# Kernel optimization log

Measured on AMD Instinct MI355X. Metric: run time of the kernel, lower is better.

Reference implementation:

```python
import jax, jax.numpy as jnp
import numpy as np

B, T, D, H, HD, FF, L, M = 2, 1024, 1024, 16, 64, 4096, 4, 128


def _ln(x, g, b):
    m = x.mean(-1, keepdims=True)
    v = ((x - m) ** 2).mean(-1, keepdims=True)
    return (x - m) * jax.lax.rsqrt(v + 1e-5) * g + b


def _rope(x, cos, sin):
    # x: (B,H,T,HD) viewed as interleaved (even,odd) pairs, as in torch Rotary
    xp = x.reshape(x.shape[:-1] + (HD // 2, 2))
    x1, x2 = xp[..., 0], xp[..., 1]
    even = x1 * cos - x2 * sin
    odd = x1 * sin + x2 * cos
    return jnp.stack([even, odd], -1).reshape(x.shape)


def setup_inputs() -> dict:
    key = jax.random.key(0)
    ks = iter(jax.random.split(key, 16))

    def n(shape, s=0.02):
        return jax.random.normal(next(ks), shape, jnp.float32) * s

    return {
        'x': jax.random.normal(next(ks), (B, T, D), jnp.float32),
        'context': jax.random.normal(next(ks), (B, T, D), jnp.float32),
        'W_in': n((D, D)), 'b_in': jnp.zeros((D,), jnp.float32),
        'ln_in_g': jnp.ones((D,), jnp.float32), 'ln_in_b': jnp.zeros((D,), jnp.float32),
        'ln1_g': jnp.ones((L, D), jnp.float32), 'ln1_b': jnp.zeros((L, D), jnp.float32),
        'Wqkv': n((L, D, 3 * D)), 'bqkv': jnp.zeros((L, 3 * D), jnp.float32),
        'Wproj': n((L, D, D)), 'bproj': jnp.zeros((L, D), jnp.float32),
        'rel_bias': n((L, 2 * M + 1, H)),
        'ln2_g': jnp.ones((L, D), jnp.float32), 'ln2_b': jnp.zeros((L, D), jnp.float32),
        'Wfc1': n((L, D, 2 * FF)), 'bfc1': jnp.zeros((L, 2 * FF), jnp.float32),
        'Wfc2': n((L, FF, D)), 'bfc2': jnp.zeros((L, D), jnp.float32),
        'ln_f_g': jnp.ones((D,), jnp.float32), 'ln_f_b': jnp.zeros((D,), jnp.float32),
        'W_out': n((D, D)), 'b_out': jnp.zeros((D,), jnp.float32),
        'alpha': jnp.array([0.3], jnp.float32),
        'beta': jnp.zeros((1,), jnp.float32),
        'alpha_scale': jnp.array([0.5], jnp.float32),
        'beta_scale': jnp.array([0.1], jnp.float32),
    }


def reference(x, context, W_in, b_in, ln_in_g, ln_in_b, ln1_g, ln1_b, Wqkv, bqkv,
              Wproj, bproj, rel_bias, ln2_g, ln2_b, Wfc1, bfc1, Wfc2, bfc2,
              ln_f_g, ln_f_b, W_out, b_out, alpha, beta, alpha_scale, beta_scale):
    scale = HD ** -0.5
    # Rotary cache (replicates the torch code's emb=cat(freqs,freqs) then
    # view(T, HD//2, 2)[...,0] quirk exactly)
    t = jnp.arange(T, dtype=jnp.float32)
    inv_freq = 1.0 / (10000.0 ** (jnp.arange(0, HD, 2, dtype=jnp.float32) / HD))
    emb = jnp.concatenate([jnp.outer(t, inv_freq)] * 2, -1)  # (T, HD)
    cos = jnp.cos(emb).reshape(T, HD // 2, 2)[..., 0]        # (T, HD/2)
    sin = jnp.sin(emb).reshape(T, HD // 2, 2)[..., 0]
    # relative-position index (T,T), clamped to [-M, M]
    idx = jnp.arange(T)
    rel = jnp.clip(idx[None, :] - idx[:, None], -M, M) + M

    h = _ln(x @ W_in + b_in + context, ln_in_g, ln_in_b)

    def step(h, p):
        g1, b1, wqkv, bq, wp, bp, rb, g2, b2, w1, bf1, w2, bf2 = p
        hn = _ln(h, g1, b1)
        qkv = (hn @ wqkv + bq).reshape(B, T, 3, H, HD)
        q = jnp.moveaxis(qkv[:, :, 0], 1, 2)   # (B,H,T,HD)
        k = jnp.moveaxis(qkv[:, :, 1], 1, 2)
        v = jnp.moveaxis(qkv[:, :, 2], 1, 2)
        q = _rope(q, cos, sin)
        k = _rope(k, cos, sin)
        bias = rb[rel].transpose(2, 0, 1)      # (H,T,T)
        attn = jax.nn.softmax(jnp.einsum('bhqd,bhkd->bhqk', q, k) * scale + bias[None], -1)
        out = jnp.einsum('bhqk,bhkd->bhqd', attn, v)
        out = jnp.moveaxis(out, 1, 2).reshape(B, T, D) @ wp + bp
        h = h + out
        hn2 = _ln(h, g2, b2)
        ab = hn2 @ w1 + bf1
        a, gate = ab[..., :FF], ab[..., FF:]
        h = h + (a * jax.nn.gelu(gate, approximate=False)) @ w2 + bf2
        return h, None

    h, _ = jax.lax.scan(step, h, (ln1_g, ln1_b, Wqkv, bqkv, Wproj, bproj, rel_bias,
                                  ln2_g, ln2_b, Wfc1, bfc1, Wfc2, bfc2))
    h = _ln(h, ln_f_g, ln_f_b)
    o = h @ W_out + b_out
    # MotionAmplifier
    a_s = jnp.clip(alpha_scale, 0.0, 1.0)
    ms = jnp.linalg.norm(o, axis=-1, keepdims=True)
    sc = 1.0 + alpha * a_s * jnp.minimum(ms, 5.0)
    return jnp.clip(o * sc + beta * beta_scale, -10.0, 10.0) + o
```

## Files before the change

### kernel.cpp

```cpp
#include <hip/hip_runtime.h>
#include <cmath>

#define B_  2
#define T_  1024
#define D_  1024
#define H_  16
#define HD_ 64
#define FF_ 4096
#define L_  4
#define M_  128

typedef __bf16 bf16x8 __attribute__((ext_vector_type(8)));
typedef __bf16 bf16x4 __attribute__((ext_vector_type(4)));
typedef float f32x4 __attribute__((ext_vector_type(4)));

__device__ __forceinline__ void async16(const void* g, void* l) {
    __builtin_amdgcn_global_load_lds(
        (const __attribute__((address_space(1))) unsigned int*)g,
        (__attribute__((address_space(3))) unsigned int*)l, 16, 0, 0);
}

template<int BM, typename CT>
__global__ __launch_bounds__(256) void gemm_bf16(
    const __bf16* __restrict__ A, const __bf16* __restrict__ Wt,
    const float* __restrict__ bias, const float* __restrict__ res,
    CT* __restrict__ C, int M, int N, int K)
{
    constexpr int MI = BM / 32;
    __shared__ alignas(16) __bf16 As[BM * 32];
    __shared__ alignas(16) __bf16 Bs[128 * 32];

    const int tid  = threadIdx.x;
    const int lane = tid & 63;
    const int wave = tid >> 6;
    const int wm   = wave & 1;
    const int wn   = wave >> 1;
    const int quad = lane >> 4;
    const int l16  = lane & 15;
    const int m0   = blockIdx.y * BM;
    const int n0   = blockIdx.x * 128;

    f32x4 acc[MI][4];
    #pragma unroll
    for (int i = 0; i < MI; i++)
        #pragma unroll
        for (int j = 0; j < 4; j++) acc[i][j] = (f32x4){0.f, 0.f, 0.f, 0.f};

    for (int k0 = 0; k0 < K; k0 += 32) {
        #pragma unroll
        for (int i = 0; i < BM / 64; i++) {
            int off = (i * 256 + tid) * 16;
            int row = off >> 6, chunk = (off >> 4) & 3;
            int gcol = (chunk ^ ((row >> 1) & 3)) * 8;
            async16(A + (size_t)(m0 + row) * K + k0 + gcol,
                    (char*)As + i * 4096 + wave * 1024);
        }
        #pragma unroll
        for (int i = 0; i < 2; i++) {
            int off = (i * 256 + tid) * 16;
            int row = off >> 6, chunk = (off >> 4) & 3;
            int gcol = (chunk ^ ((row >> 1) & 3)) * 8;
            async16(Wt + (size_t)(n0 + row) * K + k0 + gcol,
                    (char*)Bs + i * 4096 + wave * 1024);
        }
        __syncthreads();

        bf16x8 af[MI], bfr[4];
        #pragma unroll
        for (int mi = 0; mi < MI; mi++) {
            int r = wm * (BM / 2) + mi * 16 + l16;
            af[mi] = *(const bf16x8*)((const char*)As + r * 64 + (quad ^ ((r >> 1) & 3)) * 16);
        }
        #pragma unroll
        for (int ni = 0; ni < 4; ni++) {
            int r = wn * 64 + ni * 16 + l16;
            bfr[ni] = *(const bf16x8*)((const char*)Bs + r * 64 + (quad ^ ((r >> 1) & 3)) * 16);
        }
        #pragma unroll
        for (int mi = 0; mi < MI; mi++)
            #pragma unroll
            for (int ni = 0; ni < 4; ni++)
                acc[mi][ni] = __builtin_amdgcn_mfma_f32_16x16x32_bf16(
                    af[mi], bfr[ni], acc[mi][ni], 0, 0, 0);
        __syncthreads();
    }

    #pragma unroll
    for (int mi = 0; mi < MI; mi++) {
        #pragma unroll
        for (int ni = 0; ni < 4; ni++) {
            int col = n0 + wn * 64 + ni * 16 + l16;
            #pragma unroll
            for (int r = 0; r < 4; r++) {
                int row = m0 + wm * (BM / 2) + mi * 16 + quad * 4 + r;
                float v = acc[mi][ni][r] + bias[col];
                if (res) v += res[(size_t)row * N + col];
                C[(size_t)row * N + col] = (CT)v;
            }
        }
    }
}

__global__ __launch_bounds__(256) void transpose_w_kernel(
    const float* __restrict__ W, __bf16* __restrict__ Wt, int K, int N)
{
    __shared__ __bf16 t[64][80];
    int n0 = blockIdx.x * 64, k0 = blockIdx.y * 64;
    int tid = threadIdx.x;
    int r = tid >> 2, cb = (tid & 3) * 16;
    const float* src = W + (size_t)(k0 + r) * N + n0 + cb;
    #pragma unroll
    for (int j = 0; j < 16; j += 4) {
        f32x4 v = *(const f32x4*)(src + j);
        #pragma unroll
        for (int u = 0; u < 4; u++) t[cb + j + u][r] = (__bf16)v[u];
    }
    __syncthreads();
    __bf16* dst = Wt + (size_t)(n0 + r) * K + k0 + cb;
    *(bf16x8*)(dst)     = *(const bf16x8*)&t[r][cb];
    *(bf16x8*)(dst + 8) = *(const bf16x8*)&t[r][cb + 8];
}

__global__ __launch_bounds__(256) void cvt_bf16_kernel(
    const float* __restrict__ in, __bf16* __restrict__ out)
{
    size_t i = ((size_t)blockIdx.x * 256 + threadIdx.x) * 8;
    f32x4 a = *(const f32x4*)(in + i);
    f32x4 b = *(const f32x4*)(in + i + 4);
    bf16x8 o;
    #pragma unroll
    for (int u = 0; u < 4; u++) { o[u] = (__bf16)a[u]; o[4 + u] = (__bf16)b[u]; }
    *(bf16x8*)(out + i) = o;
}

template<typename OT>
__global__ __launch_bounds__(256) void ln_kernel(
    const float* __restrict__ in,
    const float* __restrict__ g, const float* __restrict__ b,
    OT* __restrict__ out)
{
    int row = blockIdx.x;
    int t = threadIdx.x;
    __shared__ float red[256];
    __shared__ float red2[256];
    const float* ip = in + (size_t)row * D_;
    float v[4];
    float sum = 0.f, sumsq = 0.f;
    #pragma unroll
    for (int j = 0; j < 4; j++) {
        int c = t + j * 256;
        float x = ip[c];
        v[j] = x;
        sum += x; sumsq += x * x;
    }
    red[t] = sum; red2[t] = sumsq;
    __syncthreads();
    for (int s = 128; s > 0; s >>= 1) {
        if (t < s) { red[t] += red[t + s]; red2[t] += red2[t + s]; }
        __syncthreads();
    }
    float mean = red[0] * (1.0f / D_);
    float var  = red2[0] * (1.0f / D_) - mean * mean;
    float rstd = rsqrtf(var + 1e-5f);
    #pragma unroll
    for (int j = 0; j < 4; j++) {
        int c = t + j * 256;
        out[(size_t)row * D_ + c] = (OT)((v[j] - mean) * rstd * g[c] + b[c]);
    }
}

__global__ __launch_bounds__(256) void repack_kernel(
    const float* __restrict__ qkv, __bf16* __restrict__ qp,
    __bf16* __restrict__ kp, __bf16* __restrict__ vp)
{
    int bh = blockIdx.y; int h = bh & (H_ - 1); int b = bh >> 4;
    int t0 = blockIdx.x * 64;
    int tid = threadIdx.x;
    __shared__ float vt[64][65];

    int r  = tid >> 2;
    int tg = t0 + r;
    int pb = (tid & 3) * 8;
    #pragma unroll
    for (int j = 0; j < 8; j++) {
        int p = pb + j;
        int jj = (2 * p) & 31;
        float f = expf(-(float)jj * (9.210340371976184f / 32.0f));
        float ang = (float)tg * f;
        float c = cosf(ang), s = sinf(ang);
        const float2 xq = *(const float2*)(qkv + ((size_t)(b * T_ + tg) * 3 + 0) * D_ + h * HD_ + 2 * p);
        size_t oq = ((size_t)bh * T_ + tg) * HD_ + 2 * p;
        qp[oq]     = (__bf16)(xq.x * c - xq.y * s);
        qp[oq + 1] = (__bf16)(xq.x * s + xq.y * c);
        const float2 xk = *(const float2*)(qkv + ((size_t)(b * T_ + tg) * 3 + 1) * D_ + h * HD_ + 2 * p);
        kp[oq]     = (__bf16)(xk.x * c - xk.y * s);
        kp[oq + 1] = (__bf16)(xk.x * s + xk.y * c);
    }
    {
        int cb = (tid & 3) * 16;
        const float* vsrc = qkv + ((size_t)(b * T_ + tg) * 3 + 2) * D_ + h * HD_ + cb;
        #pragma unroll
        for (int j = 0; j < 16; j += 4) {
            f32x4 v = *(const f32x4*)(vsrc + j);
            #pragma unroll
            for (int u = 0; u < 4; u++) vt[cb + j + u][r] = v[u];
        }
    }
    __syncthreads();
    {
        int d = tid >> 2, cb = (tid & 3) * 16;
        bf16x8 o0, o1;
        #pragma unroll
        for (int u = 0; u < 8; u++) { o0[u] = (__bf16)vt[d][cb + u]; o1[u] = (__bf16)vt[d][cb + 8 + u]; }
        __bf16* dst = vp + ((size_t)bh * HD_ + d) * T_ + t0 + cb;
        *(bf16x8*)(dst) = o0;
        *(bf16x8*)(dst + 8) = o1;
    }
}

__global__ __launch_bounds__(256) void attn_mfma_kernel(
    const __bf16* __restrict__ qp, const __bf16* __restrict__ kp,
    const __bf16* __restrict__ vp, const float* __restrict__ rb,
    __bf16* __restrict__ out)
{
    int bh = blockIdx.y; int h = bh & (H_ - 1); int b = bh >> 4;
    int q0 = blockIdx.x * 64;
    int tid = threadIdx.x;
    int lane = tid & 63, wave = tid >> 6;
    int quad = lane >> 4, l16 = lane & 15;

    __shared__ alignas(16) __bf16 Qs[64 * 64];
    __shared__ alignas(16) __bf16 Ks[64 * 64];
    __shared__ alignas(16) __bf16 Vs[64 * 64];
    __shared__ __bf16 Ps[4][16][72];
    __shared__ float rbs[2 * M_ + 1];

    for (int i = tid; i < 2 * M_ + 1; i += 256) rbs[i] = rb[i * H_ + h];

    #pragma unroll
    for (int i = 0; i < 2; i++) {
        int off = (i * 256 + tid) * 16;
        int row = off >> 7, chunk = (off >> 4) & 7;
        int gcol = (chunk ^ (row & 7)) * 8;
        async16(qp + ((size_t)bh * T_ + q0 + row) * HD_ + gcol,
                (char*)Qs + i * 4096 + wave * 1024);
    }
    __syncthreads();

    bf16x8 qfrag[2];
    {
        int r = wave * 16 + l16;
        qfrag[0] = *(const bf16x8*)((const char*)Qs + r * 128 + ((quad)     ^ (r & 7)) * 16);
        qfrag[1] = *(const bf16x8*)((const char*)Qs + r * 128 + ((4 + quad) ^ (r & 7)) * 16);
    }

    float m_run[4], l_run[4];
    f32x4 o_acc[4];
    #pragma unroll
    for (int r2 = 0; r2 < 4; r2++) { m_run[r2] = -1e30f; l_run[r2] = 0.f; }
    #pragma unroll
    for (int ni = 0; ni < 4; ni++) o_acc[ni] = (f32x4){0.f, 0.f, 0.f, 0.f};

    const int row_l  = quad * 4;
    const int qrow_g = q0 + wave * 16 + row_l;

    for (int k0 = 0; k0 < T_; k0 += 64) {
        __syncthreads();
        #pragma unroll
        for (int i = 0; i < 2; i++) {
            int off = (i * 256 + tid) * 16;
            int row = off >> 7, chunk = (off >> 4) & 7;
            int gcol = (chunk ^ (row & 7)) * 8;
            async16(kp + ((size_t)bh * T_ + k0 + row) * HD_ + gcol,
                    (char*)Ks + i * 4096 + wave * 1024);
            async16(vp + ((size_t)bh * HD_ + row) * T_ + k0 + gcol,
                    (char*)Vs + i * 4096 + wave * 1024);
        }
        __syncthreads();

        f32x4 s_acc[4];
        #pragma unroll
        for (int ni = 0; ni < 4; ni++) s_acc[ni] = (f32x4){0.f, 0.f, 0.f, 0.f};
        #pragma unroll
        for (int ni = 0; ni < 4; ni++) {
            int r = ni * 16 + l16;
            bf16x8 kf0 = *(const bf16x8*)((const char*)Ks + r * 128 + ((quad)     ^ (r & 7)) * 16);
            bf16x8 kf1 = *(const bf16x8*)((const char*)Ks + r * 128 + ((4 + quad) ^ (r & 7)) * 16);
            s_acc[ni] = __builtin_amdgcn_mfma_f32_16x16x32_bf16(qfrag[0], kf0, s_acc[ni], 0, 0, 0);
            s_acc[ni] = __builtin_amdgcn_mfma_f32_16x16x32_bf16(qfrag[1], kf1, s_acc[ni], 0, 0, 0);
        }

        float sv[4][4];
        float rmax[4] = {-1e30f, -1e30f, -1e30f, -1e30f};
        #pragma unroll
        for (int ni = 0; ni < 4; ni++) {
            int colg = k0 + ni * 16 + l16;
            #pragma unroll
            for (int r2 = 0; r2 < 4; r2++) {
                int rel = colg - (qrow_g + r2);
                rel = (rel < -M_) ? -M_ : (rel > M_ ? M_ : rel);
                float s = s_acc[ni][r2] * 0.125f + rbs[rel + M_];
                sv[ni][r2] = s;
                rmax[r2] = fmaxf(rmax[r2], s);
            }
        }
        #pragma unroll
        for (int r2 = 0; r2 < 4; r2++)
            #pragma unroll
            for (int off = 1; off < 16; off <<= 1)
                rmax[r2] = fmaxf(rmax[r2], __shfl_xor(rmax[r2], off, 64));

        float alpha[4], rsum[4];
        #pragma unroll
        for (int r2 = 0; r2 < 4; r2++) {
            float mn = fmaxf(m_run[r2], rmax[r2]);
            alpha[r2] = __expf(m_run[r2] - mn);
            m_run[r2] = mn;
            rsum[r2] = 0.f;
        }
        #pragma unroll
        for (int ni = 0; ni < 4; ni++)
            #pragma unroll
            for (int r2 = 0; r2 < 4; r2++) {
                float p = __expf(sv[ni][r2] - m_run[r2]);
                rsum[r2] += p;
                Ps[wave][row_l + r2][ni * 16 + l16] = (__bf16)p;
            }
        #pragma unroll
        for (int r2 = 0; r2 < 4; r2++) {
            #pragma unroll
            for (int off = 1; off < 16; off <<= 1)
                rsum[r2] += __shfl_xor(rsum[r2], off, 64);
            l_run[r2] = l_run[r2] * alpha[r2] + rsum[r2];
        }
        #pragma unroll
        for (int ni = 0; ni < 4; ni++)
            #pragma unroll
            for (int r2 = 0; r2 < 4; r2++) o_acc[ni][r2] *= alpha[r2];

        #pragma unroll
        for (int kk = 0; kk < 2; kk++) {
            bf16x8 pfrag = *(const bf16x8*)&Ps[wave][l16][kk * 32 + quad * 8];
            #pragma unroll
            for (int ni = 0; ni < 4; ni++) {
                int r = ni * 16 + l16;
                bf16x8 vfrag = *(const bf16x8*)((const char*)Vs + r * 128 + ((kk * 4 + quad) ^ (r & 7)) * 16);
                o_acc[ni] = __builtin_amdgcn_mfma_f32_16x16x32_bf16(pfrag, vfrag, o_acc[ni], 0, 0, 0);
            }
        }
    }

    #pragma unroll
    for (int ni = 0; ni < 4; ni++) {
        int colg = h * HD_ + ni * 16 + l16;
        #pragma unroll
        for (int r2 = 0; r2 < 4; r2++) {
            int rowg = qrow_g + r2;
            out[(size_t)(b * T_ + rowg) * D_ + colg] = (__bf16)(o_acc[ni][r2] / l_run[r2]);
        }
    }
}

__global__ __launch_bounds__(256) void glu_kernel(
    const __bf16* __restrict__ ab, __bf16* __restrict__ cc)
{
    size_t i8 = (size_t)blockIdx.x * 256 + threadIdx.x;
    size_t m = i8 >> 9;
    size_t fb = (i8 & 511) * 8;
    bf16x8 a8 = *(const bf16x8*)(ab + m * (2 * FF_) + fb);
    bf16x8 g8 = *(const bf16x8*)(ab + m * (2 * FF_) + FF_ + fb);
    bf16x8 o;
    #pragma unroll
    for (int u = 0; u < 8; u++) {
        float a = (float)a8[u];
        float g = (float)g8[u];
        float ge = 0.5f * g * (1.0f + erff(g * 0.7071067811865475f));
        o[u] = (__bf16)(a * ge);
    }
    *(bf16x8*)(cc + m * FF_ + fb) = o;
}

__global__ __launch_bounds__(256) void final_kernel(
    const float* __restrict__ o, const float* __restrict__ alpha,
    const float* __restrict__ beta, const float* __restrict__ alpha_scale,
    const float* __restrict__ beta_scale, float* __restrict__ outp)
{
    int row = blockIdx.x;
    int t = threadIdx.x;
    __shared__ float red[256];
    const float* op = o + (size_t)row * D_;
    float v[4];
    float sumsq = 0.f;
    #pragma unroll
    for (int j = 0; j < 4; j++) {
        float x = op[t + j * 256];
        v[j] = x;
        sumsq += x * x;
    }
    red[t] = sumsq; __syncthreads();
    for (int s = 128; s > 0; s >>= 1) {
        if (t < s) red[t] += red[t + s];
        __syncthreads();
    }
    float ms = sqrtf(red[0]);
    float as = fminf(fmaxf(alpha_scale[0], 0.f), 1.f);
    float sc = 1.0f + alpha[0] * as * fminf(ms, 5.0f);
    float bb = beta[0] * beta_scale[0];
    #pragma unroll
    for (int j = 0; j < 4; j++) {
        float x = v[j] * sc + bb;
        x = fminf(fmaxf(x, -10.f), 10.f);
        outp[(size_t)row * D_ + t + j * 256] = x + v[j];
    }
}

extern "C" void kernel_launch(void* const* d_in, const int* in_sizes, int n_in,
                              void* d_out, int out_size, void* d_ws, size_t ws_size,
                              hipStream_t stream)
{
    const float* x        = (const float*)d_in[0];
    const float* context  = (const float*)d_in[1];
    const float* W_in     = (const float*)d_in[2];
    const float* b_in     = (const float*)d_in[3];
    const float* ln_in_g  = (const float*)d_in[4];
    const float* ln_in_b  = (const float*)d_in[5];
    const float* ln1_g    = (const float*)d_in[6];
    const float* ln1_b    = (const float*)d_in[7];
    const float* Wqkv     = (const float*)d_in[8];
    const float* bqkv     = (const float*)d_in[9];
    const float* Wproj    = (const float*)d_in[10];
    const float* bproj    = (const float*)d_in[11];
    const float* rel_bias = (const float*)d_in[12];
    const float* ln2_g    = (const float*)d_in[13];
    const float* ln2_b    = (const float*)d_in[14];
    const float* Wfc1     = (const float*)d_in[15];
    const float* bfc1     = (const float*)d_in[16];
    const float* Wfc2     = (const float*)d_in[17];
    const float* bfc2     = (const float*)d_in[18];
    const float* ln_f_g   = (const float*)d_in[19];
    const float* ln_f_b   = (const float*)d_in[20];
    const float* W_out    = (const float*)d_in[21];
    const float* b_out    = (const float*)d_in[22];
    const float* alpha    = (const float*)d_in[23];
    const float* beta     = (const float*)d_in[24];
    const float* alpha_s  = (const float*)d_in[25];
    const float* beta_s   = (const float*)d_in[26];

    float* ws = (float*)d_ws;
    const size_t MLN = 1024 * 1024;
    const int MROWS = B_ * T_;

    float*  h    = ws;
    float*  big  = ws + 2 * MLN;
    __bf16* abb  = (__bf16*)big;
    __bf16* ccb  = (__bf16*)(ws + 10 * MLN);
    __bf16* hnb  = (__bf16*)(ws + 14 * MLN + MLN / 4);
    __bf16* abuf = (__bf16*)(ws + 15 * MLN + MLN / 4);
    __bf16* qpk  = (__bf16*)(ws + 16 * MLN + MLN / 4);
    __bf16* kpk  = (__bf16*)(ws + 17 * MLN + MLN / 4);
    __bf16* vpk  = (__bf16*)(ws + 18 * MLN + MLN / 4);
    __bf16* wtb  = (__bf16*)(ws + 19 * MLN + MLN / 4);
    __bf16* wt_qkv  = wtb;
    __bf16* wt_proj = wtb + 3145728;
    __bf16* wt_fc1  = wtb + 4194304;
    __bf16* wt_fc2  = wtb + 12582912;

    dim3 blk(256);

    cvt_bf16_kernel<<<dim3(1024), blk, 0, stream>>>(x, abuf);
    transpose_w_kernel<<<dim3(16, 16), blk, 0, stream>>>(W_in, wtb, D_, D_);
    gemm_bf16<64, float><<<dim3(8, 32), blk, 0, stream>>>(abuf, wtb, b_in, context, big,
                                                          MROWS, D_, D_);
    ln_kernel<float><<<dim3(MROWS), blk, 0, stream>>>(big, ln_in_g, ln_in_b, h);

    for (int l = 0; l < L_; l++) {
        const float* wqkv = Wqkv + (size_t)l * D_ * 3 * D_;
        const float* bq   = bqkv + (size_t)l * 3 * D_;
        const float* wp   = Wproj + (size_t)l * D_ * D_;
        const float* bp   = bproj + (size_t)l * D_;
        const float* rb   = rel_bias + (size_t)l * (2 * M_ + 1) * H_;
        const float* w1   = Wfc1 + (size_t)l * D_ * 2 * FF_;
        const float* bf1  = bfc1 + (size_t)l * 2 * FF_;
        const float* w2   = Wfc2 + (size_t)l * FF_ * D_;
        const float* bf2  = bfc2 + (size_t)l * D_;

        transpose_w_kernel<<<dim3(48, 16),  blk, 0, stream>>>(wqkv, wt_qkv, D_, 3 * D_);
        transpose_w_kernel<<<dim3(16, 16),  blk, 0, stream>>>(wp,   wt_proj, D_, D_);
        transpose_w_kernel<<<dim3(128, 16), blk, 0, stream>>>(w1,   wt_fc1, D_, 2 * FF_);
        transpose_w_kernel<<<dim3(16, 64),  blk, 0, stream>>>(w2,   wt_fc2, FF_, D_);

        ln_kernel<__bf16><<<dim3(MROWS), blk, 0, stream>>>(h, ln1_g + l * D_, ln1_b + l * D_, hnb);
        gemm_bf16<128, float><<<dim3(24, 16), blk, 0, stream>>>(hnb, wt_qkv, bq, nullptr, big,
                                                                MROWS, 3 * D_, D_);
        repack_kernel<<<dim3(T_ / 64, B_ * H_), blk, 0, stream>>>(big, qpk, kpk, vpk);
        attn_mfma_kernel<<<dim3(T_ / 64, B_ * H_), blk, 0, stream>>>(qpk, kpk, vpk, rb, abuf);
        gemm_bf16<64, float><<<dim3(8, 32), blk, 0, stream>>>(abuf, wt_proj, bp, h, h,
                                                              MROWS, D_, D_);
        ln_kernel<__bf16><<<dim3(MROWS), blk, 0, stream>>>(h, ln2_g + l * D_, ln2_b + l * D_, hnb);
        gemm_bf16<128, __bf16><<<dim3(64, 16), blk, 0, stream>>>(hnb, wt_fc1, bf1, nullptr, abb,
                                                                 MROWS, 2 * FF_, D_);
        glu_kernel<<<dim3(4096), blk, 0, stream>>>(abb, ccb);
        gemm_bf16<64, float><<<dim3(8, 32), blk, 0, stream>>>(ccb, wt_fc2, bf2, h, h,
                                                              MROWS, D_, FF_);
    }

    ln_kernel<__bf16><<<dim3(MROWS), blk, 0, stream>>>(h, ln_f_g, ln_f_b, hnb);
    transpose_w_kernel<<<dim3(16, 16), blk, 0, stream>>>(W_out, wtb, D_, D_);
    gemm_bf16<64, float><<<dim3(8, 32), blk, 0, stream>>>(hnb, wtb, b_out, nullptr, big,
                                                          MROWS, D_, D_);
    final_kernel<<<dim3(MROWS), blk, 0, stream>>>(big, alpha, beta, alpha_s, beta_s,
                                                  (float*)d_out);
}
```

Before: 1.450 ms.

## Fuse FC1 with GLU, deepen GEMM K-tile, bf16 QKV, batch weight transposes

```diff
diff --git a/kernel.cpp b/kernel.cpp
--- a/kernel.cpp
+++ b/kernel.cpp
@@ -20,15 +20,16 @@
         (__attribute__((address_space(3))) unsigned int*)l, 16, 0, 0);
 }
 
-template<int BM, typename CT>
+template<int BM, int BN, typename CT>
 __global__ __launch_bounds__(256) void gemm_bf16(
     const __bf16* __restrict__ A, const __bf16* __restrict__ Wt,
     const float* __restrict__ bias, const float* __restrict__ res,
     CT* __restrict__ C, int M, int N, int K)
 {
     constexpr int MI = BM / 32;
-    __shared__ alignas(16) __bf16 As[BM * 32];
-    __shared__ alignas(16) __bf16 Bs[128 * 32];
+    constexpr int NI = BN / 32;
+    __shared__ alignas(16) __bf16 As[BM * 64];
+    __shared__ alignas(16) __bf16 Bs[BN * 64];
 
     const int tid  = threadIdx.x;
     const int lane = tid & 63;
@@ -38,58 +39,68 @@
     const int quad = lane >> 4;
     const int l16  = lane & 15;
     const int m0   = blockIdx.y * BM;
-    const int n0   = blockIdx.x * 128;
-
-    f32x4 acc[MI][4];
+    const int n0   = blockIdx.x * BN;
+
+    f32x4 acc[MI][NI];
     #pragma unroll
     for (int i = 0; i < MI; i++)
         #pragma unroll
-        for (int j = 0; j < 4; j++) acc[i][j] = (f32x4){0.f, 0.f, 0.f, 0.f};
-
-    for (int k0 = 0; k0 < K; k0 += 32) {
-        #pragma unroll
-        for (int i = 0; i < BM / 64; i++) {
+        for (int j = 0; j < NI; j++) acc[i][j] = (f32x4){0.f, 0.f, 0.f, 0.f};
+
+    for (int k0 = 0; k0 < K; k0 += 64) {
+        #pragma unroll
+        for (int i = 0; i < BM / 32; i++) {
             int off = (i * 256 + tid) * 16;
-            int row = off >> 6, chunk = (off >> 4) & 3;
-            int gcol = (chunk ^ ((row >> 1) & 3)) * 8;
+            int row = off >> 7, chunk = (off >> 4) & 7;
+            int gcol = (chunk ^ (row & 7)) * 8;
             async16(A + (size_t)(m0 + row) * K + k0 + gcol,
                     (char*)As + i * 4096 + wave * 1024);
         }
         #pragma unroll
-        for (int i = 0; i < 2; i++) {
+        for (int i = 0; i < BN / 32; i++) {
             int off = (i * 256 + tid) * 16;
-            int row = off >> 6, chunk = (off >> 4) & 3;
-            int gcol = (chunk ^ ((row >> 1) & 3)) * 8;
+            int row = off >> 7, chunk = (off >> 4) & 7;
+            int gcol = (chunk ^ (row & 7)) * 8;
             async16(Wt + (size_t)(n0 + row) * K + k0 + gcol,
                     (char*)Bs + i * 4096 + wave * 1024);
         }
         __syncthreads();
 
-        bf16x8 af[MI], bfr[4];
+        bf16x8 af[MI][2], bfr[NI][2];
         #pragma unroll
         for (int mi = 0; mi < MI; mi++) {
             int r = wm * (BM / 2) + mi * 16 + l16;
-            af[mi] = *(const bf16x8*)((const char*)As + r * 64 + (quad ^ ((r >> 1) & 3)) * 16);
-        }
-        #pragma unroll
-        for (int ni = 0; ni < 4; ni++) {
-            int r = wn * 64 + ni * 16 + l16;
-            bfr[ni] = *(const bf16x8*)((const char*)Bs + r * 64 + (quad ^ ((r >> 1) & 3)) * 16);
-        }
-        #pragma unroll
-        for (int mi = 0; mi < MI; mi++)
-            #pragma unroll
-            for (int ni = 0; ni < 4; ni++)
-                acc[mi][ni] = __builtin_amdgcn_mfma_f32_16x16x32_bf16(
-                    af[mi], bfr[ni], acc[mi][ni], 0, 0, 0);
+            #pragma unroll
+            for (int kk = 0; kk < 2; kk++) {
+                int c = kk * 4 + quad;
+                af[mi][kk] = *(const bf16x8*)((const char*)As + r * 128 + ((c ^ (r & 7)) * 16));
+            }
+        }
+        #pragma unroll
+        for (int ni = 0; ni < NI; ni++) {
+            int r = wn * (BN / 2) + ni * 16 + l16;
+            #pragma unroll
+            for (int kk = 0; kk < 2; kk++) {
+                int c = kk * 4 + quad;
+                bfr[ni][kk] = *(const bf16x8*)((const char*)Bs + r * 128 + ((c ^ (r & 7)) * 16));
+            }
+        }
+        #pragma unroll
+        for (int kk = 0; kk < 2; kk++)
+            #pragma unroll
+            for (int mi = 0; mi < MI; mi++)
+                #pragma unroll
+                for (int ni = 0; ni < NI; ni++)
+                    acc[mi][ni] = __builtin_amdgcn_mfma_f32_16x16x32_bf16(
+                        af[mi][kk], bfr[ni][kk], acc[mi][ni], 0, 0, 0);
         __syncthreads();
     }
 
     #pragma unroll
     for (int mi = 0; mi < MI; mi++) {
         #pragma unroll
-        for (int ni = 0; ni < 4; ni++) {
-            int col = n0 + wn * 64 + ni * 16 + l16;
+        for (int ni = 0; ni < NI; ni++) {
+            int col = n0 + wn * (BN / 2) + ni * 16 + l16;
             #pragma unroll
             for (int r = 0; r < 4; r++) {
                 int row = m0 + wm * (BM / 2) + mi * 16 + quad * 4 + r;
@@ -101,9 +112,108 @@
     }
 }
 
+__global__ __launch_bounds__(256) void fc1_glu_kernel(
+    const __bf16* __restrict__ A, const __bf16* __restrict__ Wt,
+    const float* __restrict__ bias, __bf16* __restrict__ cc, int K)
+{
+    __shared__ alignas(16) __bf16 As[64 * 64];
+    __shared__ alignas(16) __bf16 Bs[128 * 64];
+    __shared__ alignas(16) __bf16 Gs[128 * 64];
+
+    const int tid  = threadIdx.x;
+    const int lane = tid & 63;
+    const int wave = tid >> 6;
+    const int wm   = wave & 1;
+    const int wn   = wave >> 1;
+    const int quad = lane >> 4;
+    const int l16  = lane & 15;
+    const int m0   = blockIdx.y * 64;
+    const int n0   = blockIdx.x * 128;
+
+    f32x4 acc_a[2][4], acc_g[2][4];
+    #pragma unroll
+    for (int i = 0; i < 2; i++)
+        #pragma unroll
+        for (int j = 0; j < 4; j++) {
+            acc_a[i][j] = (f32x4){0.f, 0.f, 0.f, 0.f};
+            acc_g[i][j] = (f32x4){0.f, 0.f, 0.f, 0.f};
+        }
+
+    for (int k0 = 0; k0 < K; k0 += 64) {
+        #pragma unroll
+        for (int i = 0; i < 2; i++) {
+            int off = (i * 256 + tid) * 16;
+            int row = off >> 7, chunk = (off >> 4) & 7;
+            int gcol = (chunk ^ (row & 7)) * 8;
+            async16(A + (size_t)(m0 + row) * K + k0 + gcol,
+                    (char*)As + i * 4096 + wave * 1024);
+        }
+        #pragma unroll
+        for (int i = 0; i < 4; i++) {
+            int off = (i * 256 + tid) * 16;
+            int row = off >> 7, chunk = (off >> 4) & 7;
+            int gcol = (chunk ^ (row & 7)) * 8;
+            async16(Wt + (size_t)(n0 + row) * K + k0 + gcol,
+                    (char*)Bs + i * 4096 + wave * 1024);
+            async16(Wt + (size_t)(FF_ + n0 + row) * K + k0 + gcol,
+                    (char*)Gs + i * 4096 + wave * 1024);
+        }
+        __syncthreads();
+
+        bf16x8 af[2][2];
+        #pragma unroll
+        for (int mi = 0; mi < 2; mi++) {
+            int r = wm * 32 + mi * 16 + l16;
+            #pragma unroll
+            for (int kk = 0; kk < 2; kk++) {
+                int c = kk * 4 + quad;
+                af[mi][kk] = *(const bf16x8*)((const char*)As + r * 128 + ((c ^ (r & 7)) * 16));
+            }
+        }
+        #pragma unroll
+        for (int kk = 0; kk < 2; kk++) {
+            #pragma unroll
+            for (int ni = 0; ni < 4; ni++) {
+                int r = wn * 64 + ni * 16 + l16;
+                int c = kk * 4 + quad;
+                bf16x8 b1 = *(const bf16x8*)((const char*)Bs + r * 128 + ((c ^ (r & 7)) * 16));
+                bf16x8 b2 = *(const bf16x8*)((const char*)Gs + r * 128 + ((c ^ (r & 7)) * 16));
+                #pragma unroll
+                for (int mi = 0; mi < 2; mi++) {
+                    acc_a[mi][ni] = __builtin_amdgcn_mfma_f32_16x16x32_bf16(
+                        af[mi][kk], b1, acc_a[mi][ni], 0, 0, 0);
+                    acc_g[mi][ni] = __builtin_amdgcn_mfma_f32_16x16x32_bf16(
+                        af[mi][kk], b2, acc_g[mi][ni], 0, 0, 0);
+                }
+            }
+        }
+        __syncthreads();
+    }
+
+    #pragma unroll
+    for (int mi = 0; mi < 2; mi++) {
+        #pragma unroll
+        for (int ni = 0; ni < 4; ni++) {
+            int col = n0 + wn * 64 + ni * 16 + l16;
+            float ba = bias[col], bg = bias[FF_ + col];
+            #pragma unroll
+            for (int r = 0; r < 4; r++) {
+                int row = m0 + wm * 32 + mi * 16 + quad * 4 + r;
+                float a = acc_a[mi][ni][r] + ba;
+                float g = acc_g[mi][ni][r] + bg;
+                float ge = 0.5f * g * (1.0f + erff(g * 0.7071067811865475f));
+                cc[(size_t)row * FF_ + col] = (__bf16)(a * ge);
+            }
+        }
+    }
+}
+
 __global__ __launch_bounds__(256) void transpose_w_kernel(
-    const float* __restrict__ W, __bf16* __restrict__ Wt, int K, int N)
-{
+    const float* __restrict__ W, __bf16* __restrict__ Wt, int K, int N,
+    size_t dstride)
+{
+    W  += (size_t)blockIdx.z * K * N;
+    Wt += (size_t)blockIdx.z * dstride;
     __shared__ __bf16 t[64][80];
     int n0 = blockIdx.x * 64, k0 = blockIdx.y * 64;
     int tid = threadIdx.x;
@@ -170,49 +280,55 @@
 }
 
 __global__ __launch_bounds__(256) void repack_kernel(
-    const float* __restrict__ qkv, __bf16* __restrict__ qp,
+    const __bf16* __restrict__ qkv, __bf16* __restrict__ qp,
     __bf16* __restrict__ kp, __bf16* __restrict__ vp)
 {
     int bh = blockIdx.y; int h = bh & (H_ - 1); int b = bh >> 4;
     int t0 = blockIdx.x * 64;
     int tid = threadIdx.x;
-    __shared__ float vt[64][65];
+    __shared__ __bf16 vt[64][72];
 
     int r  = tid >> 2;
     int tg = t0 + r;
-    int pb = (tid & 3) * 8;
-    #pragma unroll
-    for (int j = 0; j < 8; j++) {
-        int p = pb + j;
-        int jj = (2 * p) & 31;
+    int cb = (tid & 3) * 16;
+
+    const __bf16* qsrc = qkv + ((size_t)(b * T_ + tg) * 3 + 0) * D_ + h * HD_ + cb;
+    const __bf16* ksrc = qkv + ((size_t)(b * T_ + tg) * 3 + 1) * D_ + h * HD_ + cb;
+    bf16x8 q0 = *(const bf16x8*)qsrc,  q1 = *(const bf16x8*)(qsrc + 8);
+    bf16x8 k0 = *(const bf16x8*)ksrc,  k1 = *(const bf16x8*)(ksrc + 8);
+    bf16x8 qo0, qo1, ko0, ko1;
+    #pragma unroll
+    for (int p = 0; p < 8; p++) {
+        int pg = (cb >> 1) + p;
+        int jj = (2 * pg) & 31;
         float f = expf(-(float)jj * (9.210340371976184f / 32.0f));
         float ang = (float)tg * f;
         float c = cosf(ang), s = sinf(ang);
-        const float2 xq = *(const float2*)(qkv + ((size_t)(b * T_ + tg) * 3 + 0) * D_ + h * HD_ + 2 * p);
-        size_t oq = ((size_t)bh * T_ + tg) * HD_ + 2 * p;
-        qp[oq]     = (__bf16)(xq.x * c - xq.y * s);
-        qp[oq + 1] = (__bf16)(xq.x * s + xq.y * c);
-        const float2 xk = *(const float2*)(qkv + ((size_t)(b * T_ + tg) * 3 + 1) * D_ + h * HD_ + 2 * p);
-        kp[oq]     = (__bf16)(xk.x * c - xk.y * s);
-        kp[oq + 1] = (__bf16)(xk.x * s + xk.y * c);
-    }
+        float qe, qo, ke, ko;
+        if (p < 4) { qe = (float)q0[2*p]; qo = (float)q0[2*p+1]; ke = (float)k0[2*p]; ko = (float)k0[2*p+1]; }
+        else       { qe = (float)q1[2*(p-4)]; qo = (float)q1[2*(p-4)+1]; ke = (float)k1[2*(p-4)]; ko = (float)k1[2*(p-4)+1]; }
+        float a0 = qe * c - qo * s, a1 = qe * s + qo * c;
+        float b0 = ke * c - ko * s, b1 = ke * s + ko * c;
+        if (p < 4) { qo0[2*p] = (__bf16)a0; qo0[2*p+1] = (__bf16)a1; ko0[2*p] = (__bf16)b0; ko0[2*p+1] = (__bf16)b1; }
+        else       { qo1[2*(p-4)] = (__bf16)a0; qo1[2*(p-4)+1] = (__bf16)a1; ko1[2*(p-4)] = (__bf16)b0; ko1[2*(p-4)+1] = (__bf16)b1; }
+    }
+    size_t odst = ((size_t)bh * T_ + tg) * HD_ + cb;
+    *(bf16x8*)(qp + odst) = qo0; *(bf16x8*)(qp + odst + 8) = qo1;
+    *(bf16x8*)(kp + odst) = ko0; *(bf16x8*)(kp + odst + 8) = ko1;
+
     {
-        int cb = (tid & 3) * 16;
-        const float* vsrc = qkv + ((size_t)(b * T_ + tg) * 3 + 2) * D_ + h * HD_ + cb;
-        #pragma unroll
-        for (int j = 0; j < 16; j += 4) {
-            f32x4 v = *(const f32x4*)(vsrc + j);
-            #pragma unroll
-            for (int u = 0; u < 4; u++) vt[cb + j + u][r] = v[u];
-        }
+        const __bf16* vsrc = qkv + ((size_t)(b * T_ + tg) * 3 + 2) * D_ + h * HD_ + cb;
+        bf16x8 v0 = *(const bf16x8*)vsrc, v1 = *(const bf16x8*)(vsrc + 8);
+        #pragma unroll
+        for (int u = 0; u < 8; u++) { vt[cb + u][r] = v0[u]; vt[cb + 8 + u][r] = v1[u]; }
     }
     __syncthreads();
     {
-        int d = tid >> 2, cb = (tid & 3) * 16;
+        int d = tid >> 2, cb2 = (tid & 3) * 16;
         bf16x8 o0, o1;
         #pragma unroll
-        for (int u = 0; u < 8; u++) { o0[u] = (__bf16)vt[d][cb + u]; o1[u] = (__bf16)vt[d][cb + 8 + u]; }
-        __bf16* dst = vp + ((size_t)bh * HD_ + d) * T_ + t0 + cb;
+        for (int u = 0; u < 8; u++) { o0[u] = vt[d][cb2 + u]; o1[u] = vt[d][cb2 + 8 + u]; }
+        __bf16* dst = vp + ((size_t)bh * HD_ + d) * T_ + t0 + cb2;
         *(bf16x8*)(dst) = o0;
         *(bf16x8*)(dst + 8) = o1;
     }
@@ -359,25 +475,6 @@
             out[(size_t)(b * T_ + rowg) * D_ + colg] = (__bf16)(o_acc[ni][r2] / l_run[r2]);
         }
     }
-}
-
-__global__ __launch_bounds__(256) void glu_kernel(
-    const __bf16* __restrict__ ab, __bf16* __restrict__ cc)
-{
-    size_t i8 = (size_t)blockIdx.x * 256 + threadIdx.x;
-    size_t m = i8 >> 9;
-    size_t fb = (i8 & 511) * 8;
-    bf16x8 a8 = *(const bf16x8*)(ab + m * (2 * FF_) + fb);
-    bf16x8 g8 = *(const bf16x8*)(ab + m * (2 * FF_) + FF_ + fb);
-    bf16x8 o;
-    #pragma unroll
-    for (int u = 0; u < 8; u++) {
-        float a = (float)a8[u];
-        float g = (float)g8[u];
-        float ge = 0.5f * g * (1.0f + erff(g * 0.7071067811865475f));
-        o[u] = (__bf16)(a * ge);
-    }
-    *(bf16x8*)(cc + m * FF_ + fb) = o;
 }
 
 __global__ __launch_bounds__(256) void final_kernel(
@@ -451,63 +548,65 @@
     const int MROWS = B_ * T_;
 
     float*  h    = ws;
-    float*  big  = ws + 2 * MLN;
-    __bf16* abb  = (__bf16*)big;
-    __bf16* ccb  = (__bf16*)(ws + 10 * MLN);
-    __bf16* hnb  = (__bf16*)(ws + 14 * MLN + MLN / 4);
-    __bf16* abuf = (__bf16*)(ws + 15 * MLN + MLN / 4);
-    __bf16* qpk  = (__bf16*)(ws + 16 * MLN + MLN / 4);
-    __bf16* kpk  = (__bf16*)(ws + 17 * MLN + MLN / 4);
-    __bf16* vpk  = (__bf16*)(ws + 18 * MLN + MLN / 4);
-    __bf16* wtb  = (__bf16*)(ws + 19 * MLN + MLN / 4);
-    __bf16* wt_qkv  = wtb;
-    __bf16* wt_proj = wtb + 3145728;
-    __bf16* wt_fc1  = wtb + 4194304;
-    __bf16* wt_fc2  = wtb + 12582912;
+    __bf16* hnb  = (__bf16*)(ws + 2 * MLN);
+    __bf16* abuf = (__bf16*)(ws + 3 * MLN);
+    __bf16* qpk  = (__bf16*)(ws + 4 * MLN);
+    __bf16* kpk  = (__bf16*)(ws + 5 * MLN);
+    __bf16* vpk  = (__bf16*)(ws + 6 * MLN);
+    __bf16* qkvb = (__bf16*)(ws + 8 * MLN);
+    __bf16* ccb  = (__bf16*)(ws + 12 * MLN);
+    float*  tmpf = ws + 17 * MLN;
+    __bf16* wtb  = (__bf16*)(ws + 19 * MLN);
+
+    __bf16* wt_in  = wtb;
+    __bf16* wt_out = wtb + 1048576;
+    const size_t LSTRIDE = 16777216;
+    __bf16* wt_qkv0  = wtb + 2097152;
+    __bf16* wt_proj0 = wt_qkv0 + 3145728;
+    __bf16* wt_fc10  = wt_qkv0 + 4194304;
+    __bf16* wt_fc20  = wt_qkv0 + 12582912;
 
     dim3 blk(256);
 
+    transpose_w_kernel<<<dim3(16, 16, 1),  blk, 0, stream>>>(W_in,  wt_in,  D_, D_, 0);
+    transpose_w_kernel<<<dim3(16, 16, 1),  blk, 0, stream>>>(W_out, wt_out, D_, D_, 0);
+    transpose_w_kernel<<<dim3(48, 16, 4),  blk, 0, stream>>>(Wqkv,  wt_qkv0,  D_, 3 * D_, LSTRIDE);
+    transpose_w_kernel<<<dim3(16, 16, 4),  blk, 0, stream>>>(Wproj, wt_proj0, D_, D_, LSTRIDE);
+    transpose_w_kernel<<<dim3(128, 16, 4), blk, 0, stream>>>(Wfc1,  wt_fc10,  D_, 2 * FF_, LSTRIDE);
+    transpose_w_kernel<<<dim3(16, 64, 4),  blk, 0, stream>>>(Wfc2,  wt_fc20,  FF_, D_, LSTRIDE);
+
     cvt_bf16_kernel<<<dim3(1024), blk, 0, stream>>>(x, abuf);
-    transpose_w_kernel<<<dim3(16, 16), blk, 0, stream>>>(W_in, wtb, D_, D_);
-    gemm_bf16<64, float><<<dim3(8, 32), blk, 0, stream>>>(abuf, wtb, b_in, context, big,
-                                                          MROWS, D_, D_);
-    ln_kernel<float><<<dim3(MROWS), blk, 0, stream>>>(big, ln_in_g, ln_in_b, h);
+    gemm_bf16<64, 64, float><<<dim3(16, 32), blk, 0, stream>>>(abuf, wt_in, b_in, context,
+                                                               tmpf, MROWS, D_, D_);
+    ln_kernel<float><<<dim3(MROWS), blk, 0, stream>>>(tmpf, ln_in_g, ln_in_b, h);
 
     for (int l = 0; l < L_; l++) {
-        const float* wqkv = Wqkv + (size_t)l * D_ * 3 * D_;
         const float* bq   = bqkv + (size_t)l * 3 * D_;
-        const float* wp   = Wproj + (size_t)l * D_ * D_;
         const float* bp   = bproj + (size_t)l * D_;
         const float* rb   = rel_bias + (size_t)l * (2 * M_ + 1) * H_;
-        const float* w1   = Wfc1 + (size_t)l * D_ * 2 * FF_;
         const float* bf1  = bfc1 + (size_t)l * 2 * FF_;
-        const float* w2   = Wfc2 + (size_t)l * FF_ * D_;
         const float* bf2  = bfc2 + (size_t)l * D_;
-
-        transpose_w_kernel<<<dim3(48, 16),  blk, 0, stream>>>(wqkv, wt_qkv, D_, 3 * D_);
-        transpose_w_kernel<<<dim3(16, 16),  blk, 0, stream>>>(wp,   wt_proj, D_, D_);
-        transpose_w_kernel<<<dim3(128, 16), blk, 0, stream>>>(w1,   wt_fc1, D_, 2 * FF_);
-        transpose_w_kernel<<<dim3(16, 64),  blk, 0, stream>>>(w2,   wt_fc2, FF_, D_);
+        __bf16* wt_qkv  = wt_qkv0  + (size_t)l * LSTRIDE;
+        __bf16* wt_proj = wt_proj0 + (size_t)l * LSTRIDE;
+        __bf16* wt_fc1  = wt_fc10  + (size_t)l * LSTRIDE;
+        __bf16* wt_fc2  = wt_fc20  + (size_t)l * LSTRIDE;
 
         ln_kernel<__bf16><<<dim3(MROWS), blk, 0, stream>>>(h, ln1_g + l * D_, ln1_b + l * D_, hnb);
-        gemm_bf16<128, float><<<dim3(24, 16), blk, 0, stream>>>(hnb, wt_qkv, bq, nullptr, big,
-                                                                MROWS, 3 * D_, D_);
-        repack_kernel<<<dim3(T_ / 64, B_ * H_), blk, 0, stream>>>(big, qpk, kpk, vpk);
+        gemm_bf16<64, 128, __bf16><<<dim3(24, 32), blk, 0, stream>>>(hnb, wt_qkv, bq, nullptr,
+                                                                     qkvb, MROWS, 3 * D_, D_);
+        repack_kernel<<<dim3(T_ / 64, B_ * H_), blk, 0, stream>>>(qkvb, qpk, kpk, vpk);
         attn_mfma_kernel<<<dim3(T_ / 64, B_ * H_), blk, 0, stream>>>(qpk, kpk, vpk, rb, abuf);
-        gemm_bf16<64, float><<<dim3(8, 32), blk, 0, stream>>>(abuf, wt_proj, bp, h, h,
-                                                              MROWS, D_, D_);
+        gemm_bf16<64, 64, float><<<dim3(16, 32), blk, 0, stream>>>(abuf, wt_proj, bp, h, h,
+                                                                   MROWS, D_, D_);
         ln_kernel<__bf16><<<dim3(MROWS), blk, 0, stream>>>(h, ln2_g + l * D_, ln2_b + l * D_, hnb);
-        gemm_bf16<128, __bf16><<<dim3(64, 16), blk, 0, stream>>>(hnb, wt_fc1, bf1, nullptr, abb,
-                                                                 MROWS, 2 * FF_, D_);
-        glu_kernel<<<dim3(4096), blk, 0, stream>>>(abb, ccb);
-        gemm_bf16<64, float><<<dim3(8, 32), blk, 0, stream>>>(ccb, wt_fc2, bf2, h, h,
-                                                              MROWS, D_, FF_);
+        fc1_glu_kernel<<<dim3(32, 32), blk, 0, stream>>>(hnb, wt_fc1, bf1, ccb, D_);
+        gemm_bf16<64, 64, float><<<dim3(16, 32), blk, 0, stream>>>(ccb, wt_fc2, bf2, h, h,
+                                                                   MROWS, D_, FF_);
     }
 
     ln_kernel<__bf16><<<dim3(MROWS), blk, 0, stream>>>(h, ln_f_g, ln_f_b, hnb);
-    transpose_w_kernel<<<dim3(16, 16), blk, 0, stream>>>(W_out, wtb, D_, D_);
-    gemm_bf16<64, float><<<dim3(8, 32), blk, 0, stream>>>(hnb, wtb, b_out, nullptr, big,
-                                                          MROWS, D_, D_);
-    final_kernel<<<dim3(MROWS), blk, 0, stream>>>(big, alpha, beta, alpha_s, beta_s,
+    gemm_bf16<64, 64, float><<<dim3(16, 32), blk, 0, stream>>>(hnb, wt_out, b_out, nullptr,
+                                                               tmpf, MROWS, D_, D_);
+    final_kernel<<<dim3(MROWS), blk, 0, stream>>>(tmpf, alpha, beta, alpha_s, beta_s,
                                                   (float*)d_out);
 }
```

After: 1.213 ms. -16.3%, faster.
